# Kernel optimization log

Hardware: AMD Instinct MI355X
Metric: run time of the kernel (lower is better)

## Reference

```python
import jax, jax.numpy as jnp
import numpy as np

B, C, H, W = 4, 8, 384, 384
CHANS = 18  # MLP hidden width (module default chans=18)
BAND = 32   # half-width of acquired low-frequency band


def setup_inputs() -> dict:
    key = jax.random.key(0)
    ks = jax.random.split(key, 8)
    acquired_kspace = jax.random.normal(ks[0], (B, C, H, W, 2), jnp.float32)
    acquiring_kspace = jax.random.normal(ks[1], (B, C, H, W, 2), jnp.float32)
    mid = W // 2
    am = np.zeros((B, W), np.float32)
    am[:, mid - BAND:mid + BAND] = 1.0  # acquired center band -> left/right well-defined
    acquired_mask = jnp.asarray(am)
    qm = np.zeros((B, W), np.float32)
    qm[:, ::24] = 1.0  # columns currently being acquired
    acquiring_mask = jnp.asarray(qm)
    CH = C * H
    IN = 2 * CH  # concat(acquiring_features, acquired_features)
    # MLP: Linear(IN,CHANS)+ReLU, Linear(CHANS,CHANS)+ReLU x2, Linear(CHANS,1)+Sigmoid (pools=4 layers)
    W1 = jax.random.normal(ks[2], (CHANS, IN), jnp.float32) * 0.02
    b1 = jnp.zeros((CHANS,), jnp.float32)
    W2 = jax.random.normal(ks[3], (CHANS, CHANS), jnp.float32) * 0.02
    b2 = jnp.zeros((CHANS,), jnp.float32)
    W3 = jax.random.normal(ks[4], (CHANS, CHANS), jnp.float32) * 0.02
    b3 = jnp.zeros((CHANS,), jnp.float32)
    W4 = jax.random.normal(ks[5], (1, CHANS), jnp.float32) * 0.02
    b4 = jnp.zeros((1,), jnp.float32)
    return dict(acquired_kspace=acquired_kspace, acquiring_kspace=acquiring_kspace,
                acquired_mask=acquired_mask, acquiring_mask=acquiring_mask,
                W1=W1, b1=b1, W2=W2, b2=b2, W3=W3, b3=b3, W4=W4, b4=b4)


def reference(acquired_kspace, acquiring_kspace, acquired_mask, acquiring_mask,
              W1, b1, W2, b2, W3, b3, W4, b4):
    cabs = lambda x: jnp.sqrt(jnp.sum(x * x, axis=-1))  # complex magnitude of trailing (re,im)
    # per-column flattened features, row-major over (C,H) like torch.flatten: [B, W, C*H]
    Fq = cabs(acquiring_kspace).transpose(0, 3, 1, 2).reshape(B, W, -1)
    Fa = cabs(acquired_kspace).transpose(0, 3, 1, 2).reshape(B, W, -1)
    CH = Fq.shape[-1]
    # split first linear over the concat([acquiring, acquired]) input
    Pq = Fq @ W1[:, :CH].T   # [B, W_i, CHANS]
    Pa = Fa @ W1[:, CH:].T   # [B, W_c, CHANS]
    h = jax.nn.relu(Pq[:, :, None, :] + Pa[:, None, :, :] + b1)  # [B, W_i, W_c, CHANS]
    h = jax.nn.relu(h @ W2.T + b2)
    h = jax.nn.relu(h @ W3.T + b3)
    out = jax.nn.sigmoid(h @ W4.T + b4)[..., 0]  # [B, W_i, W_c]
    # faithful left/right bounds from acquired_mask (same as torch.nonzero(...)[0][0])
    mid = W // 2
    right = mid + jnp.argmax(acquired_mask[:, mid:] < 1.0, axis=1)              # [B]
    left = jnp.argmax(acquired_mask[:, :mid][:, ::-1] < 1.0, axis=1) + 1        # [B]
    c = jnp.arange(W)
    cmask = (c[None, :] >= left[:, None]) & (c[None, :] < right[:, None])       # [B, W_c]
    denom = (right - left).astype(out.dtype)
    heat = jnp.sum(out * cmask[:, None, :].astype(out.dtype), axis=2) / denom[:, None]
    heat = jnp.where(acquiring_mask > 0, heat, jnp.zeros_like(heat))            # only nonzero acquiring cols
    return jnp.broadcast_to(heat[:, None, :], (B, H, W))  # torch.cat of h copies along dim=1
```

## Files before the change

kernel.cpp:

```cpp
#include <hip/hip_runtime.h>
#include <math.h>
#include <limits.h>

#define kB 4
#define kC 8
#define kH 384
#define kW 384
#define kCH (kC * kH)
#define kIN (2 * kCH)
#define kNC 18
#define kMID (kW / 2)

#define NCH 8
#define RPC (kCH / NCH)
#define NGRP 48
#define kN (kB * kW * kNC)

#define E18(M) M(0) M(1) M(2) M(3) M(4) M(5) M(6) M(7) M(8) M(9) M(10) M(11) M(12) M(13) M(14) M(15) M(16) M(17)
#define E12(M) M(0) M(1) M(2) M(3) M(4) M(5) M(6) M(7) M(8) M(9) M(10) M(11)

__device__ __forceinline__ void mask_bounds(const float* __restrict__ amb,
                                            int lane, int* left, int* right) {
    unsigned long long mR0 = __ballot(amb[kMID + lane] < 1.0f);
    unsigned long long mR1 = __ballot(amb[kMID + 64 + lane] < 1.0f);
    unsigned long long mR2 = __ballot(amb[kMID + 128 + lane] < 1.0f);
    unsigned long long mL0 = __ballot(amb[kMID - 1 - lane] < 1.0f);
    unsigned long long mL1 = __ballot(amb[kMID - 65 - lane] < 1.0f);
    unsigned long long mL2 = __ballot(amb[kMID - 129 - lane] < 1.0f);
    int candR = mR0 ? __builtin_ctzll(mR0)
              : (mR1 ? 64 + __builtin_ctzll(mR1)
              : (mR2 ? 128 + __builtin_ctzll(mR2) : 0));
    int candL = mL0 ? __builtin_ctzll(mL0)
              : (mL1 ? 64 + __builtin_ctzll(mL1)
              : (mL2 ? 128 + __builtin_ctzll(mL2) : 0));
    *left  = candL + 1;
    *right = kMID + candR;
}

__global__ __launch_bounds__(256)
void proj_kernel(const float* __restrict__ acquired,
                 const float* __restrict__ acquiring,
                 const float* __restrict__ am,
                 const float* __restrict__ qm,
                 const float* __restrict__ W1,
                 float* __restrict__ Pq_part, float* __restrict__ Pa_part,
                 float* __restrict__ out) {
    int g = blockIdx.x;
    int chunk = blockIdx.y & (NCH - 1);
    int pass = blockIdx.y >> 3;
    int b = blockIdx.z;
    int tid = threadIdx.x;
    int w0 = g * 8;
    int r0 = chunk * RPC;

    {
        int flatB = (blockIdx.z * gridDim.y + blockIdx.y) * gridDim.x + blockIdx.x;
        int gid = flatB * 256 + tid;
        if (gid < kB * kH * kW) {
            int w = gid % kW;
            int ob = gid / (kH * kW);
            if (!(qm[ob * kW + w] > 0.0f)) out[gid] = 0.0f;
        }
    }

    int lane = tid & 63;
    bool need;
    if (pass == 0) {
        int left, right;
        mask_bounds(am + b * kW, lane, &left, &right);
        need = (left < w0 + 8) && (right > w0);
    } else {
        bool q = qm[b * kW + w0 + (lane & 7)] > 0.0f;
        need = (__ballot(q) != 0ull);
    }
    if (!need) return;

    const float* ks = (pass == 0) ? acquired : acquiring;
    const float* w1 = (pass == 0) ? (W1 + kCH) : W1;

    int c8 = tid & 7, r32 = tid >> 3;
    int w = w0 + c8;
    int wave = tid >> 6;

    __shared__ float sW[RPC][20];
    __shared__ float sRed[4][8][kNC];

    const float* colp = ks + ((size_t)(b * kCH + r0 + r32) * kW + w) * 2;
#define KLOAD(it) const float2 v##it = *reinterpret_cast<const float2*>(colp + (size_t)(it) * 32 * kW * 2);
    E12(KLOAD)

    for (int t = tid; t < kNC * RPC; t += 256) {
        int j = t / RPC, i = t - j * RPC;
        sW[i][j] = w1[j * kIN + r0 + i];
    }
    __syncthreads();

#define KMAG(it) const float f##it = sqrtf(v##it.x * v##it.x + v##it.y * v##it.y);
    E12(KMAG)

#define PDECL(j) float a##j = 0.0f;
    E18(PDECL)

#define ROWF(it) { \
        const float* row = &sW[r32 + 32 * (it)][0]; \
        const float4 q0 = *reinterpret_cast<const float4*>(row); \
        const float4 q1 = *reinterpret_cast<const float4*>(row + 4); \
        const float4 q2 = *reinterpret_cast<const float4*>(row + 8); \
        const float4 q3 = *reinterpret_cast<const float4*>(row + 12); \
        const float2 q4 = *reinterpret_cast<const float2*>(row + 16); \
        const float f = f##it; \
        a0  = fmaf(f, q0.x, a0);  a1  = fmaf(f, q0.y, a1);  \
        a2  = fmaf(f, q0.z, a2);  a3  = fmaf(f, q0.w, a3);  \
        a4  = fmaf(f, q1.x, a4);  a5  = fmaf(f, q1.y, a5);  \
        a6  = fmaf(f, q1.z, a6);  a7  = fmaf(f, q1.w, a7);  \
        a8  = fmaf(f, q2.x, a8);  a9  = fmaf(f, q2.y, a9);  \
        a10 = fmaf(f, q2.z, a10); a11 = fmaf(f, q2.w, a11); \
        a12 = fmaf(f, q3.x, a12); a13 = fmaf(f, q3.y, a13); \
        a14 = fmaf(f, q3.z, a14); a15 = fmaf(f, q3.w, a15); \
        a16 = fmaf(f, q4.x, a16); a17 = fmaf(f, q4.y, a17); }
    E12(ROWF)

#define WRED(j) { a##j += __shfl_down(a##j, 32, 64); a##j += __shfl_down(a##j, 16, 64); \
                  a##j += __shfl_down(a##j, 8, 64); }
    E18(WRED)
    if (lane < 8) {
#define SSTORE(j) sRed[wave][lane][j] = a##j;
        E18(SSTORE)
    }
    __syncthreads();
    if (tid < 8 * kNC) {
        int c = tid / kNC, j = tid - c * kNC;
        float s = sRed[0][c][j] + sRed[1][c][j] + sRed[2][c][j] + sRed[3][c][j];
        float* Pp = (pass == 0) ? Pa_part : Pq_part;
        Pp[((size_t)chunk * kB * kW + (size_t)b * kW + (w0 + c)) * kNC + j] = s;
    }
}

__global__ __launch_bounds__(256)
void pair_kernel(const float* __restrict__ Pq_part, const float* __restrict__ Pa_part,
                 const float* __restrict__ am, const float* __restrict__ qmask,
                 const float* __restrict__ b1, const float* __restrict__ W2,
                 const float* __restrict__ b2, const float* __restrict__ W3,
                 const float* __restrict__ b3, const float* __restrict__ W4,
                 const float* __restrict__ b4, float* __restrict__ out) {
    int wi = blockIdx.x, b = blockIdx.y, tid = threadIdx.x;
    if (!(qmask[b * kW + wi] > 0.0f)) return;

    int lane = tid & 63, wave = tid >> 6;
    int left, right;
    mask_bounds(am + b * kW, lane, &left, &right);
    int span = right - left;

    __shared__ float sPa[kW][19];
    __shared__ float2 sW2[kNC * kNC / 2], sW3[kNC * kNC / 2];
    __shared__ float sW4[kNC], sb1[kNC], sb2[kNC], sb3[kNC], sPq[kNC];
    __shared__ float sb4s, wred[4], sHeat;

    if (tid < kNC * kNC / 2) {
        sW2[tid] = reinterpret_cast<const float2*>(W2)[tid];
        sW3[tid] = reinterpret_cast<const float2*>(W3)[tid];
    }
    if (tid >= 192 && tid < 192 + kNC) {
        int j = tid - 192;
        float s = 0.0f;
#pragma unroll
        for (int c = 0; c < NCH; ++c)
            s += Pq_part[((size_t)c * kB * kW + (size_t)b * kW + wi) * kNC + j];
        sPq[j] = s;
        sW4[j] = W4[j]; sb1[j] = b1[j]; sb2[j] = b2[j]; sb3[j] = b3[j];
    }
    if (tid == 255) sb4s = b4[0];

    for (int t = tid; t < span * kNC; t += 256) {
        int k = t / kNC, j = t - k * kNC;
        float s = 0.0f;
#pragma unroll
        for (int c = 0; c < NCH; ++c)
            s += Pa_part[((size_t)c * kB * kW + (size_t)b * kW + (left + k)) * kNC + j];
        sPa[k][j] = s;
    }
    __syncthreads();

#define DOT2(S, k, v) (S[(k)*9+0].x*v##0  + S[(k)*9+0].y*v##1  + \
                       S[(k)*9+1].x*v##2  + S[(k)*9+1].y*v##3  + \
                       S[(k)*9+2].x*v##4  + S[(k)*9+2].y*v##5  + \
                       S[(k)*9+3].x*v##6  + S[(k)*9+3].y*v##7  + \
                       S[(k)*9+4].x*v##8  + S[(k)*9+4].y*v##9  + \
                       S[(k)*9+5].x*v##10 + S[(k)*9+5].y*v##11 + \
                       S[(k)*9+6].x*v##12 + S[(k)*9+6].y*v##13 + \
                       S[(k)*9+7].x*v##14 + S[(k)*9+7].y*v##15 + \
                       S[(k)*9+8].x*v##16 + S[(k)*9+8].y*v##17)

    float ssum = 0.0f;
    for (int k = tid; k < span; k += 256) {
        const float* pa = &sPa[k][0];
#define L1(j) float x##j = fmaxf(sPq[j] + sb1[j] + pa[j], 0.0f);
        E18(L1)
        asm volatile("" ::: "memory");
#define L2(k) float y##k = fmaxf(sb2[k] + DOT2(sW2, k, x), 0.0f);
        E18(L2)
        asm volatile("" ::: "memory");
#define L3(k) float z##k = fmaxf(sb3[k] + DOT2(sW3, k, y), 0.0f);
        E18(L3)
        asm volatile("" ::: "memory");
        float t = sb4s +
            (sW4[0]*z0 + sW4[1]*z1 + sW4[2]*z2 + sW4[3]*z3 + sW4[4]*z4 + sW4[5]*z5 +
             sW4[6]*z6 + sW4[7]*z7 + sW4[8]*z8 + sW4[9]*z9 + sW4[10]*z10 + sW4[11]*z11 +
             sW4[12]*z12 + sW4[13]*z13 + sW4[14]*z14 + sW4[15]*z15 + sW4[16]*z16 + sW4[17]*z17);
        ssum += 1.0f / (1.0f + expf(-t));
    }

    ssum += __shfl_down(ssum, 32, 64); ssum += __shfl_down(ssum, 16, 64);
    ssum += __shfl_down(ssum,  8, 64); ssum += __shfl_down(ssum,  4, 64);
    ssum += __shfl_down(ssum,  2, 64); ssum += __shfl_down(ssum,  1, 64);
    if (lane == 0) wred[wave] = ssum;
    __syncthreads();
    if (tid == 0)
        sHeat = (wred[0] + wred[1] + wred[2] + wred[3]) / (float)span;
    __syncthreads();

    float hv = sHeat;
    for (int h = tid; h < kH; h += 256)
        out[((size_t)b * kH + h) * kW + wi] = hv;
}

extern "C" void kernel_launch(void* const* d_in, const int* in_sizes, int n_in,
                              void* d_out, int out_size, void* d_ws, size_t ws_size,
                              hipStream_t stream) {
    const float* acquired       = (const float*)d_in[0];
    const float* acquiring      = (const float*)d_in[1];
    const float* acquired_mask  = (const float*)d_in[2];
    const float* acquiring_mask = (const float*)d_in[3];
    const float* W1 = (const float*)d_in[4];
    const float* b1 = (const float*)d_in[5];
    const float* W2 = (const float*)d_in[6];
    const float* b2 = (const float*)d_in[7];
    const float* W3 = (const float*)d_in[8];
    const float* b3 = (const float*)d_in[9];
    const float* W4 = (const float*)d_in[10];
    const float* b4 = (const float*)d_in[11];
    float* out = (float*)d_out;

    float* Pa_part = (float*)d_ws;
    float* Pq_part = Pa_part + (size_t)NCH * kN;

    proj_kernel<<<dim3(NGRP, 2 * NCH, kB), 256, 0, stream>>>(
        acquired, acquiring, acquired_mask, acquiring_mask, W1, Pq_part, Pa_part, out);
    pair_kernel<<<dim3(kW, kB), 256, 0, stream>>>(
        Pq_part, Pa_part, acquired_mask, acquiring_mask,
        b1, W2, b2, W3, b3, W4, b4, out);
}
```

Measured before the change: 145.8 us.

## Compact acquiring columns into dense 8-column groups and vectorize W1 staging

In the acquiring pass, each block now takes the next eight set columns of the acquiring mask, found with ballots and popcounts, instead of a fixed run of eight adjacent columns. Previously a group was processed whenever any of its eight columns was set, so most of the loaded k-space columns were wasted work. Compaction cuts the number of active blocks and skips loads for unused columns, at the cost of scattered column loads and extra index arithmetic. W1 staging into shared memory also switches to float4 loads.

```diff
diff --git a/kernel.cpp b/kernel.cpp
--- a/kernel.cpp
+++ b/kernel.cpp
@@ -37,6 +37,20 @@
     *right = kMID + candR;
 }
 
+__device__ __forceinline__ int nth_set(const unsigned long long* m, int n) {
+#pragma unroll
+    for (int j = 0; j < 6; ++j) {
+        int p = __popcll(m[j]);
+        if (n < p) {
+            unsigned long long x = m[j];
+            for (int t = 0; t < n; ++t) x &= (x - 1);
+            return 64 * j + (int)__builtin_ctzll(x);
+        }
+        n -= p;
+    }
+    return -1;
+}
+
 __global__ __launch_bounds__(256)
 void proj_kernel(const float* __restrict__ acquired,
                  const float* __restrict__ acquiring,
@@ -50,7 +64,6 @@
     int pass = blockIdx.y >> 3;
     int b = blockIdx.z;
     int tid = threadIdx.x;
-    int w0 = g * 8;
     int r0 = chunk * RPC;
 
     {
@@ -64,34 +77,49 @@
     }
 
     int lane = tid & 63;
-    bool need;
+    int c8 = tid & 7, r32 = tid >> 3;
+    int wave = tid >> 6;
+
+    __shared__ float sW[RPC][20];
+    __shared__ float sRed[4][8][kNC];
+    __shared__ int sCol[8];
+
+    int wcol;
+    bool slot_ok;
     if (pass == 0) {
         int left, right;
         mask_bounds(am + b * kW, lane, &left, &right);
-        need = (left < w0 + 8) && (right > w0);
+        int w0 = g * 8;
+        if (!((left < w0 + 8) && (right > w0))) return;
+        wcol = w0 + c8;
+        slot_ok = true;
     } else {
-        bool q = qm[b * kW + w0 + (lane & 7)] > 0.0f;
-        need = (__ballot(q) != 0ull);
-    }
-    if (!need) return;
+        unsigned long long qmm[6];
+#pragma unroll
+        for (int j = 0; j < 6; ++j)
+            qmm[j] = __ballot(qm[b * kW + 64 * j + lane] > 0.0f);
+        int totp = 0;
+#pragma unroll
+        for (int j = 0; j < 6; ++j) totp += __popcll(qmm[j]);
+        if (8 * g >= totp) return;
+        int found = nth_set(qmm, 8 * g + c8);
+        slot_ok = (found >= 0);
+        wcol = slot_ok ? found : 0;
+    }
+    if (tid < 8) sCol[tid] = slot_ok ? wcol : -1;
 
     const float* ks = (pass == 0) ? acquired : acquiring;
     const float* w1 = (pass == 0) ? (W1 + kCH) : W1;
 
-    int c8 = tid & 7, r32 = tid >> 3;
-    int w = w0 + c8;
-    int wave = tid >> 6;
-
-    __shared__ float sW[RPC][20];
-    __shared__ float sRed[4][8][kNC];
-
-    const float* colp = ks + ((size_t)(b * kCH + r0 + r32) * kW + w) * 2;
+    const float* colp = ks + ((size_t)(b * kCH + r0 + r32) * kW + wcol) * 2;
 #define KLOAD(it) const float2 v##it = *reinterpret_cast<const float2*>(colp + (size_t)(it) * 32 * kW * 2);
     E12(KLOAD)
 
-    for (int t = tid; t < kNC * RPC; t += 256) {
-        int j = t / RPC, i = t - j * RPC;
-        sW[i][j] = w1[j * kIN + r0 + i];
+    for (int t = tid; t < kNC * (RPC / 4); t += 256) {
+        int j = t / (RPC / 4), i4 = (t - j * (RPC / 4)) * 4;
+        float4 v = *reinterpret_cast<const float4*>(&w1[j * kIN + r0 + i4]);
+        sW[i4 + 0][j] = v.x; sW[i4 + 1][j] = v.y;
+        sW[i4 + 2][j] = v.z; sW[i4 + 3][j] = v.w;
     }
     __syncthreads();
 
@@ -130,9 +158,12 @@
     __syncthreads();
     if (tid < 8 * kNC) {
         int c = tid / kNC, j = tid - c * kNC;
-        float s = sRed[0][c][j] + sRed[1][c][j] + sRed[2][c][j] + sRed[3][c][j];
-        float* Pp = (pass == 0) ? Pa_part : Pq_part;
-        Pp[((size_t)chunk * kB * kW + (size_t)b * kW + (w0 + c)) * kNC + j] = s;
+        int wc = sCol[c];
+        if (wc >= 0) {
+            float s = sRed[0][c][j] + sRed[1][c][j] + sRed[2][c][j] + sRed[3][c][j];
+            float* Pp = (pass == 0) ? Pa_part : Pq_part;
+            Pp[((size_t)chunk * kB * kW + (size_t)b * kW + wc) * kNC + j] = s;
+        }
     }
 }
 
```

After: 154.1 us. 1.06x slower.
